# Performance work log

Hardware: AMD Instinct MI355X
Metric: run time of the kernel (lower is better)

The kernel has to match this reference:

```python
import jax, jax.numpy as jnp
import numpy as np

# Config derived from init_kwargs
DIM = 256
DSTATE = 64
DCONV = 3
HEADDIM = 64
CHUNK = 256
NGROUPS = 1
DINNER = int(2.0 * DIM)                 # 512
NHEADS = DINNER // HEADDIM              # 8
CONVDIM = DINNER + 2 * NGROUPS * DSTATE  # 640 (x, B, C share the depthwise conv)
DPROJ = 2 * DINNER + 2 * NGROUPS * DSTATE + NHEADS  # z + xBC + dt


def setup_inputs() -> dict:
    key = jax.random.key(0)
    ks = jax.random.split(key, 8)
    B, H, W = 8, 64, 64
    return dict(
        x=jax.random.normal(ks[0], (B, DIM, H, W), jnp.float32),
        ln_w=jnp.ones((DIM,), jnp.float32),
        ln_b=jnp.zeros((DIM,), jnp.float32),
        in_proj_w=jax.random.normal(ks[1], (DPROJ, DIM), jnp.float32) * 0.02,
        conv_w=jax.random.normal(ks[2], (CONVDIM, 1, DCONV, DCONV), jnp.float32) * 0.1,
        conv_b=jnp.zeros((CONVDIM,), jnp.float32),
        A_log=jnp.log(jax.random.uniform(ks[3], (NHEADS,), jnp.float32, 1.0, 16.0)),
        D=jnp.ones((NHEADS,), jnp.float32),
        dt_bias=jax.random.uniform(ks[4], (NHEADS,), jnp.float32, -2.0, 0.0),
        rms_w=jnp.ones((DINNER,), jnp.float32),
        out_proj_w=jax.random.normal(ks[5], (DIM, DINNER), jnp.float32) * 0.02,
    )


def _ssd(X, dA, Bm, Cm, chunk):
    """Mamba2 SSD chunked parallel scan.
    X:  (b, l, h, p)  inputs already multiplied by dt
    dA: (b, l, h)     dt * A (negative)
    Bm, Cm: (b, l, h, n)
    """
    b, l, h, p = X.shape
    n = Bm.shape[-1]
    c = l // chunk
    q = chunk
    Xc = X.reshape(b, c, q, h, p)
    Bc = Bm.reshape(b, c, q, h, n)
    Cc = Cm.reshape(b, c, q, h, n)
    Ac = dA.reshape(b, c, q, h).transpose(0, 3, 1, 2)            # (b,h,c,q)
    Acs = jnp.cumsum(Ac, axis=-1)                                # (b,h,c,q)
    # intra-chunk (diagonal blocks): causal decay matrix L
    tri = jnp.tril(jnp.ones((q, q), bool))
    Ldec = jnp.where(tri, jnp.exp(Acs[..., :, None] - Acs[..., None, :]), 0.0)
    Y_diag = jnp.einsum('bcqhn,bcshn,bhcqs,bcshp->bcqhp', Cc, Bc, Ldec, Xc)
    # per-chunk final states
    decay_states = jnp.exp(Acs[..., -1:] - Acs)                  # (b,h,c,q)
    states = jnp.einsum('bcqhn,bhcq,bcqhp->bchpn', Bc, decay_states, Xc)
    # inter-chunk recurrence (segment-sum over chunk totals)
    A_last = jnp.pad(Acs[..., -1], ((0, 0), (0, 0), (1, 0)))     # (b,h,c+1)
    ccs = jnp.cumsum(A_last, axis=-1)
    tric = jnp.tril(jnp.ones((c + 1, c + 1), bool))
    decay_chunk = jnp.where(tric, jnp.exp(ccs[..., :, None] - ccs[..., None, :]), 0.0)
    states0 = jnp.concatenate([jnp.zeros_like(states[:, :1]), states], axis=1)
    prev = jnp.einsum('bhzc,bchpn->bzhpn', decay_chunk, states0)[:, :-1]
    # contribution of carried-in state (off-diagonal blocks)
    Y_off = jnp.einsum('bcqhn,bchpn,bhcq->bcqhp', Cc, prev, jnp.exp(Acs))
    return (Y_diag + Y_off).reshape(b, l, h, p)


def _forward(x, ln_w, ln_b, in_proj_w, conv_w, conv_b, A_log, D, dt_bias, rms_w, out_proj_w):
    Bn, Cd, Hh, Ww = x.shape
    L = Hh * Ww
    # LayerNorm over channel dim (channel-first LayerNorm2d)
    mu = jnp.mean(x, axis=1, keepdims=True)
    var = jnp.mean((x - mu) ** 2, axis=1, keepdims=True)
    xn = (x - mu) * jax.lax.rsqrt(var + 1e-5)
    xn = xn * ln_w[None, :, None, None] + ln_b[None, :, None, None]
    # input projection (1x1): -> z | xBC | dt
    zxbcdt = jnp.einsum('bchw,dc->bdhw', xn, in_proj_w)
    z = zxbcdt[:, :DINNER]
    xBC = zxbcdt[:, DINNER:DINNER + CONVDIM]
    dt = zxbcdt[:, DINNER + CONVDIM:]                            # (b, nheads, H, W)
    # depthwise 2D conv + SiLU on xBC
    xBC = jax.lax.conv_general_dilated(
        xBC, conv_w, (1, 1), 'SAME',
        dimension_numbers=('NCHW', 'OIHW', 'NCHW'), feature_group_count=CONVDIM)
    xBC = jax.nn.silu(xBC + conv_b[None, :, None, None])
    # flatten spatial -> sequence, channel-last
    def to_seq(t):
        return t.reshape(Bn, t.shape[1], L).transpose(0, 2, 1)
    xBC, dt, z = to_seq(xBC), to_seq(dt), to_seq(z)
    xs = xBC[..., :DINNER].reshape(Bn, L, NHEADS, HEADDIM)
    Bg = xBC[..., DINNER:DINNER + NGROUPS * DSTATE].reshape(Bn, L, NGROUPS, DSTATE)
    Cg = xBC[..., DINNER + NGROUPS * DSTATE:].reshape(Bn, L, NGROUPS, DSTATE)
    hpg = NHEADS // NGROUPS
    Bm = jnp.repeat(Bg, hpg, axis=2)
    Cm = jnp.repeat(Cg, hpg, axis=2)
    dt = jax.nn.softplus(dt + dt_bias[None, None, :])            # (b, L, nheads)
    A = -jnp.exp(A_log)
    y = _ssd(xs * dt[..., None], dt * A[None, None, :], Bm, Cm, CHUNK)
    y = y + D[None, None, :, None] * xs                          # skip connection
    y = y.reshape(Bn, L, DINNER)
    # gated RMSNorm: norm(y * silu(z)) * w
    y = y * jax.nn.silu(z)
    y = y * jax.lax.rsqrt(jnp.mean(y * y, axis=-1, keepdims=True) + 1e-5) * rms_w
    out = jnp.einsum('bld,cd->blc', y, out_proj_w)
    out = out.transpose(0, 2, 1).reshape(Bn, Cd, Hh, Ww)
    return x + out                                               # residual


def reference(x, ln_w, ln_b, in_proj_w, conv_w, conv_b, A_log, D, dt_bias, rms_w, out_proj_w):
    return _forward(x, ln_w, ln_b, in_proj_w, conv_w, conv_b, A_log, D, dt_bias, rms_w, out_proj_w)
```

## Files before the change

### kernel.cpp

```cpp
#include <hip/hip_runtime.h>
#include <hip/hip_bf16.h>
#include <math.h>

#define DIMC   256
#define LSP    4096
#define BATCH  8
#define DINNER 512
#define NHEADS 8
#define HEADDIM 64
#define DSTATE 64
#define CONVDIM 640
#define DPROJ  1160
#define MPAD   1280
#define CHUNK  256
#define NCHUNK 16

typedef unsigned short u16;
typedef __attribute__((ext_vector_type(8))) unsigned short u16x8;
typedef __attribute__((ext_vector_type(8))) short s16x8;
typedef __attribute__((ext_vector_type(4))) float f32x4;

#define MFMA16(a,b,c) __builtin_amdgcn_mfma_f32_16x16x32_bf16((s16x8)(a),(s16x8)(b),(c),0,0,0)

__device__ __forceinline__ float bf2f(u16 u){ return __uint_as_float(((unsigned int)u)<<16); }
__device__ __forceinline__ u16 f2bf(float f){
  unsigned int x = __float_as_uint(f);
  unsigned int r = (x + 0x7fffu + ((x>>16)&1u)) >> 16;
  return (u16)r;
}
__device__ __forceinline__ float softplusf(float x){ return (x > 20.f) ? x : __logf(1.f + __expf(x)); }
__device__ __forceinline__ float siluf(float x){ return x * __builtin_amdgcn_rcpf(1.f + __expf(-x)); }

__global__ void convert_w(const float* __restrict__ src, u16* __restrict__ dst,
                          int total, int valid){
  int i = blockIdx.x*256 + threadIdx.x;
  if (i >= total) return;
  dst[i] = (i < valid) ? f2bf(src[i]) : (u16)0;
}

__global__ void convert_w_rms(const float* __restrict__ src, const float* __restrict__ rmsw,
                              u16* __restrict__ dst){
  int i = blockIdx.x*256 + threadIdx.x;
  if (i >= DIMC*DINNER) return;
  dst[i] = f2bf(src[i] * rmsw[i & (DINNER-1)]);
}

__global__ void ln_kernel(const float* __restrict__ X, const float* __restrict__ lnw,
                          const float* __restrict__ lnb, u16* __restrict__ XNT) {
  int pos = blockIdx.x*256 + threadIdx.x;
  int b = pos >> 12, l = pos & (LSP-1);
  const float* xb = X + ((size_t)b*DIMC)*LSP + l;
  float sum=0.f, sq=0.f;
  for (int c=0;c<DIMC;c++){ float v=xb[(size_t)c*LSP]; sum+=v; sq+=v*v; }
  float mu = sum*(1.f/DIMC);
  float var = sq*(1.f/DIMC) - mu*mu;
  float rs = rsqrtf(var + 1e-5f);
  u16* ob = XNT + ((size_t)(b*LSP + l))*DIMC;
  for (int c0=0;c0<DIMC;c0+=8){
    u16x8 v8;
    #pragma unroll
    for(int j=0;j<8;j++){
      float v = xb[(size_t)(c0+j)*LSP];
      v8[j] = f2bf((v-mu)*rs*lnw[c0+j] + lnb[c0+j]);
    }
    *(u16x8*)&ob[c0] = v8;
  }
}

__global__ __launch_bounds__(256,2) void gemm_in_fused(
    const u16* __restrict__ W, const u16* __restrict__ XNT,
    u16* __restrict__ ZT, u16* __restrict__ XBC, u16* __restrict__ DT){
  __shared__ u16 Xs[128][264];
  __shared__ u16 Ws[128][32];
  int tid=threadIdx.x, w=tid>>6, lane=tid&63, l15=lane&15, quad=lane>>4;
  int n0=blockIdx.x*128, mh=blockIdx.y, b=blockIdx.z;
  {
    const u16* src = XNT + ((size_t)(b*LSP + n0))*DIMC;
    #pragma unroll
    for (int i=0;i<16;i++){
      int g = i*256 + tid;
      int row = g>>5, c8 = (g&31)*8;
      *(u16x8*)&Xs[row][c8] = *(const u16x8*)&src[(size_t)row*DIMC + c8];
    }
  }
  for (int pti=0; pti<5; pti++){
    int ptg = mh*5 + pti;
    int m0 = ptg*128;
    f32x4 acc[4][4];
    #pragma unroll
    for(int i=0;i<4;i++)
      #pragma unroll
      for(int j=0;j<4;j++) acc[i][j]=(f32x4){0.f,0.f,0.f,0.f};
    for (int k0=0;k0<DIMC;k0+=32){
      __syncthreads();
      {
        int ch = tid*2;
        int r = ch>>2, o=(ch&3)*8;
        *(u16x8*)&Ws[r][o] = *(const u16x8*)&W[(size_t)(m0+r)*DIMC + k0 + o];
        ch++; r = ch>>2; o=(ch&3)*8;
        *(u16x8*)&Ws[r][o] = *(const u16x8*)&W[(size_t)(m0+r)*DIMC + k0 + o];
      }
      __syncthreads();
      u16x8 af[4], bfr[4];
      if (ptg < 4){
        #pragma unroll
        for(int mt=0;mt<4;mt++) af[mt] = *(const u16x8*)&Xs[(w>>1)*64+mt*16+l15][k0+quad*8];
        #pragma unroll
        for(int nt=0;nt<4;nt++) bfr[nt] = *(const u16x8*)&Ws[(w&1)*64+nt*16+l15][quad*8];
      } else {
        #pragma unroll
        for(int mt=0;mt<4;mt++) af[mt] = *(const u16x8*)&Ws[(w>>1)*64+mt*16+l15][quad*8];
        #pragma unroll
        for(int nt=0;nt<4;nt++) bfr[nt] = *(const u16x8*)&Xs[(w&1)*64+nt*16+l15][k0+quad*8];
      }
      #pragma unroll
      for(int mt=0;mt<4;mt++)
        #pragma unroll
        for(int nt=0;nt<4;nt++)
          acc[mt][nt]=MFMA16(af[mt],bfr[nt],acc[mt][nt]);
    }
    if (ptg < 4){
      #pragma unroll
      for(int mt=0;mt<4;mt++)
        #pragma unroll
        for(int nt=0;nt<4;nt++)
          #pragma unroll
          for(int r=0;r<4;r++){
            int lrow = n0 + (w>>1)*64 + mt*16 + quad*4 + r;
            int dcol = m0 + (w&1)*64 + nt*16 + l15;
            ZT[((size_t)b*LSP + lrow)*DINNER + dcol] = f2bf(acc[mt][nt][r]);
          }
    } else {
      #pragma unroll
      for(int mt=0;mt<4;mt++)
        #pragma unroll
        for(int nt=0;nt<4;nt++)
          #pragma unroll
          for(int r=0;r<4;r++){
            int prow = m0 + (w>>1)*64 + mt*16 + quad*4 + r;
            if (prow>=DPROJ) continue;
            int col = n0 + (w&1)*64 + nt*16 + l15;
            u16 v = f2bf(acc[mt][nt][r]);
            if (prow<DINNER+CONVDIM)  XBC[((size_t)b*CONVDIM+(prow-DINNER))*LSP+col]=v;
            else                      DT[((size_t)b*NHEADS+(prow-DINNER-CONVDIM))*LSP+col]=v;
          }
    }
  }
}

__global__ void gemm_out_mfma(const u16* __restrict__ A, const u16* __restrict__ Bm,
                              const float* __restrict__ Res, float* __restrict__ Out){
  __shared__ u16 As[128][32];
  __shared__ u16 Bs[128][32];
  __shared__ float rinv[128];
  int tid=threadIdx.x, w=tid>>6, lane=tid&63, l15=lane&15, quad=lane>>4;
  int b=blockIdx.z, m0=blockIdx.y*128, n0=blockIdx.x*128;
  const u16* Bb = Bm + ((size_t)b*LSP + n0)*DINNER;
  for (int rr=w; rr<128; rr+=4){
    u16x8 v = *(const u16x8*)&Bb[(size_t)rr*DINNER + lane*8];
    float s=0.f;
    #pragma unroll
    for(int j=0;j<8;j++){ float f=bf2f(v[j]); s+=f*f; }
    #pragma unroll
    for(int o=32;o>0;o>>=1) s += __shfl_xor(s,o,64);
    if (lane==0) rinv[rr] = rsqrtf(s*(1.f/DINNER) + 1e-5f);
  }
  f32x4 acc[4][4];
  #pragma unroll
  for(int i=0;i<4;i++)
    #pragma unroll
    for(int j=0;j<4;j++) acc[i][j] = (f32x4){0.f,0.f,0.f,0.f};
  for (int k0=0;k0<DINNER;k0+=32){
    __syncthreads();
    {
      int ch = tid*2;
      int r = ch>>2, o=(ch&3)*8;
      *(u16x8*)&As[r][o] = *(const u16x8*)&A[(size_t)(m0+r)*DINNER + k0 + o];
      *(u16x8*)&Bs[r][o] = *(const u16x8*)&Bb[(size_t)r*DINNER + k0 + o];
      ch++; r = ch>>2; o=(ch&3)*8;
      *(u16x8*)&As[r][o] = *(const u16x8*)&A[(size_t)(m0+r)*DINNER + k0 + o];
      *(u16x8*)&Bs[r][o] = *(const u16x8*)&Bb[(size_t)r*DINNER + k0 + o];
    }
    __syncthreads();
    u16x8 af[4], bfr[4];
    #pragma unroll
    for(int mt=0;mt<4;mt++) af[mt] = *(const u16x8*)&As[(w>>1)*64+mt*16+l15][quad*8];
    #pragma unroll
    for(int nt=0;nt<4;nt++) bfr[nt] = *(const u16x8*)&Bs[(w&1)*64+nt*16+l15][quad*8];
    #pragma unroll
    for(int mt=0;mt<4;mt++)
      #pragma unroll
      for(int nt=0;nt<4;nt++)
        acc[mt][nt]=MFMA16(af[mt],bfr[nt],acc[mt][nt]);
  }
  #pragma unroll
  for(int mt=0;mt<4;mt++)
    #pragma unroll
    for(int nt=0;nt<4;nt++){
      float rv = rinv[(w&1)*64 + nt*16 + l15];
      #pragma unroll
      for(int r=0;r<4;r++){
        int row = m0 + (w>>1)*64 + mt*16 + quad*4 + r;
        int col = n0 + (w&1)*64 + nt*16 + l15;
        size_t oi = ((size_t)b*DIMC+row)*LSP+col;
        Out[oi] = acc[mt][nt][r]*rv + Res[oi];
      }
    }
}

__global__ void conv_kernel(u16* __restrict__ XBC, const float* __restrict__ CW,
                            const float* __restrict__ CB){
  int ch = blockIdx.x, b = blockIdx.y, tid = threadIdx.x;
  __shared__ float plane[66*66];
  u16* base = XBC + ((size_t)b*CONVDIM + ch)*LSP;
  for (int idx=tid; idx<66*66; idx+=256){
    int yy = idx/66 - 1, xx = idx%66 - 1;
    float v = 0.f;
    if (yy>=0 && yy<64 && xx>=0 && xx<64) v = bf2f(base[yy*64+xx]);
    plane[idx] = v;
  }
  float wg[9];
  #pragma unroll
  for (int t=0;t<9;t++) wg[t] = CW[ch*9+t];
  float bias = CB[ch];
  __syncthreads();
  for (int r=0;r<16;r++){
    int pix = tid + r*256;
    int y = pix>>6, x = pix&63;
    float s=0.f;
    #pragma unroll
    for(int dy=0;dy<3;dy++)
      #pragma unroll
      for(int dx=0;dx<3;dx++) s += plane[(y+dy)*66 + x+dx]*wg[dy*3+dx];
    base[pix] = f2bf(siluf(s + bias));
  }
}

__global__ void ssd_pre_kernel(const u16* __restrict__ DT, const float* __restrict__ A_log,
                               const float* __restrict__ dt_bias, float* __restrict__ ACS,
                               float* __restrict__ DTV, float* __restrict__ DASUM){
  int c=blockIdx.x, h=blockIdx.y, b=blockIdx.z, tid=threadIdx.x;
  __shared__ float acs[CHUNK];
  size_t base = ((size_t)b*NHEADS+h)*LSP + c*CHUNK + tid;
  float raw = bf2f(DT[base]);
  float dtv = softplusf(raw + dt_bias[h]);
  float Ah = -__expf(A_log[h]);
  acs[tid] = dtv*Ah;
  __syncthreads();
  for(int o=1;o<256;o<<=1){
    float add=(tid>=o)?acs[tid-o]:0.f;
    __syncthreads(); acs[tid]+=add; __syncthreads();
  }
  ACS[base] = acs[tid];
  DTV[base] = dtv;
  if (tid==CHUNK-1) DASUM[((size_t)b*NHEADS+h)*NCHUNK+c] = acs[tid];
}

__global__ __launch_bounds__(256,4) void ssd_states_mfma(
    const float* __restrict__ ACS, const float* __restrict__ DTV,
    const float* __restrict__ DASUM, const u16* __restrict__ XBC,
    float* __restrict__ STATES){
  int c=blockIdx.x, h=blockIdx.y, b=blockIdx.z;
  int tid=threadIdx.x, w=tid>>6, lane=tid&63, l15=lane&15, quad=lane>>4;
  __shared__ float wdt[CHUNK];
  __shared__ u16 Xw[64][136];
  __shared__ u16 Bn[64][136];
  {
    size_t base = ((size_t)b*NHEADS+h)*LSP + c*CHUNK + tid;
    float atot = DASUM[((size_t)b*NHEADS+h)*NCHUNK+c];
    wdt[tid] = DTV[base]*__expf(atot - ACS[base]);
  }
  __syncthreads();
  f32x4 acc[4];
  #pragma unroll
  for(int i=0;i<4;i++) acc[i] = (f32x4){0.f,0.f,0.f,0.f};
  size_t cb = (size_t)c*CHUNK;
  for(int th=0; th<2; th++){
    __syncthreads();
    {
      int n=tid&63, q4=tid>>6;
      const u16* Xg = XBC + ((size_t)b*CONVDIM + h*HEADDIM + n)*LSP + cb + th*128;
      const u16* Bg = XBC + ((size_t)b*CONVDIM + DINNER + n)*LSP + cb + th*128;
      #pragma unroll
      for(int i=0;i<4;i++){
        int o = q4*32+i*8;
        u16x8 v = *(const u16x8*)&Xg[o];
        u16x8 wv;
        #pragma unroll
        for(int j=0;j<8;j++) wv[j]=f2bf(bf2f(v[j])*wdt[th*128+o+j]);
        *(u16x8*)&Xw[n][o]=wv;
        *(u16x8*)&Bn[n][o] = *(const u16x8*)&Bg[o];
      }
    }
    __syncthreads();
    #pragma unroll
    for(int k8=0;k8<4;k8++){
      u16x8 a = *(const u16x8*)&Xw[w*16+l15][k8*32+quad*8];
      #pragma unroll
      for(int nt=0;nt<4;nt++){
        u16x8 bb = *(const u16x8*)&Bn[nt*16+l15][k8*32+quad*8];
        acc[nt]=MFMA16(a,bb,acc[nt]);
      }
    }
  }
  float* dst = STATES + (((size_t)b*NHEADS+h)*NCHUNK+c)*4096;
  #pragma unroll
  for(int nt=0;nt<4;nt++)
    #pragma unroll
    for(int r=0;r<4;r++)
      dst[(w*16+quad*4+r)*64 + nt*16+l15] = acc[nt][r];
}

__global__ void ssd_scan_kernel(const float* __restrict__ STATES, const float* __restrict__ DASUM,
                                u16* __restrict__ PREVB){
  int g = blockIdx.x, h = blockIdx.y, b = blockIdx.z, tid = threadIdx.x;
  int e = g*256 + tid;
  size_t hb = (size_t)b*NHEADS + h;
  size_t base = hb*NCHUNK*4096 + e;
  float s = 0.f;
  for (int cc=0;cc<NCHUNK;cc++){
    PREVB[base + (size_t)cc*4096] = f2bf(s);
    s = s*__expf(DASUM[hb*NCHUNK + cc]) + STATES[base + (size_t)cc*4096];
  }
}

__global__ __launch_bounds__(256,4) void ssd_y_mfma(
    const float* __restrict__ ACS, const float* __restrict__ DTV,
    const u16* __restrict__ XBC, const float* __restrict__ Dp,
    const u16* __restrict__ PREVB, const u16* __restrict__ ZT,
    u16* __restrict__ YG){
  int bx = blockIdx.x; int c = bx>>2, tb = bx&3;
  int h = blockIdx.y, b = blockIdx.z;
  int tid=threadIdx.x, w=tid>>6, lane=tid&63, l15=lane&15, quad=lane>>4;
  __shared__ float acs[CHUNK];
  __shared__ float dtv[CHUNK];
  __shared__ u16 Ct[64][72];
  __shared__ u16 Bsb[64][72];
  __shared__ u16 Xsb[64][72];
  __shared__ u16 P[4][16][72];
  {
    size_t base = ((size_t)b*NHEADS+h)*LSP + c*CHUNK + tid;
    acs[tid] = ACS[base];
    dtv[tid] = DTV[base];
  }
  {
    int n = tid&63, q4 = tid>>6;
    const u16* Cg = XBC + ((size_t)b*CONVDIM + DINNER + DSTATE + n)*LSP + (size_t)c*CHUNK + tb*64;
    #pragma unroll
    for(int i=0;i<2;i++){
      u16x8 v = *(const u16x8*)&Cg[q4*16+i*8];
      #pragma unroll
      for(int j=0;j<8;j++) Ct[q4*16+i*8+j][n]=v[j];
    }
  }
  __syncthreads();
  f32x4 Yd[4], Yo[4];
  #pragma unroll
  for(int i=0;i<4;i++){ Yd[i]=(f32x4){0.f,0.f,0.f,0.f}; Yo[i]=(f32x4){0.f,0.f,0.f,0.f}; }
  int trow = w*16 + l15;
  u16x8 ca0 = *(const u16x8*)&Ct[trow][quad*8];
  u16x8 ca1 = *(const u16x8*)&Ct[trow][32+quad*8];
  {
    const u16* Pg = PREVB + (((size_t)b*NHEADS+h)*NCHUNK + c)*4096;
    #pragma unroll
    for(int pt=0;pt<4;pt++){
      u16x8 b0 = *(const u16x8*)&Pg[(pt*16+l15)*64 + quad*8];
      u16x8 b1 = *(const u16x8*)&Pg[(pt*16+l15)*64 + 32 + quad*8];
      Yo[pt]=MFMA16(ca0,b0,Yo[pt]);
      Yo[pt]=MFMA16(ca1,b1,Yo[pt]);
    }
  }
  int tloc = tb*64 + w*16 + quad*4;
  float acst[4];
  #pragma unroll
  for(int r=0;r<4;r++) acst[r] = acs[tloc+r];
  float Dh = Dp[h];
  for(int sb=0; sb<=tb; sb++){
    __syncthreads();
    {
      int n=tid&63, q4=tid>>6;
      const u16* Bg = XBC + ((size_t)b*CONVDIM + DINNER + n)*LSP + (size_t)c*CHUNK + sb*64;
      #pragma unroll
      for(int i=0;i<2;i++){
        u16x8 v = *(const u16x8*)&Bg[q4*16+i*8];
        #pragma unroll
        for(int j=0;j<8;j++) Bsb[q4*16+i*8+j][n]=v[j];
      }
      const u16* Xg = XBC + ((size_t)b*CONVDIM + h*HEADDIM + n)*LSP + (size_t)c*CHUNK + sb*64;
      #pragma unroll
      for(int i=0;i<2;i++){
        int o = q4*16+i*8;
        *(u16x8*)&Xsb[n][o] = *(const u16x8*)&Xg[o];
      }
    }
    __syncthreads();
    f32x4 S[4];
    #pragma unroll
    for(int st=0;st<4;st++){
      S[st]=(f32x4){0.f,0.f,0.f,0.f};
      u16x8 b0 = *(const u16x8*)&Bsb[st*16+l15][quad*8];
      u16x8 b1 = *(const u16x8*)&Bsb[st*16+l15][32+quad*8];
      S[st]=MFMA16(ca0,b0,S[st]);
      S[st]=MFMA16(ca1,b1,S[st]);
    }
    if (sb < tb){
      #pragma unroll
      for(int st=0;st<4;st++){
        int s = sb*64 + st*16 + l15;
        float as = acs[s], dv = dtv[s];
        #pragma unroll
        for(int r=0;r<4;r++)
          P[w][quad*4+r][st*16+l15] = f2bf(S[st][r]*__expf(acst[r]-as)*dv);
      }
    } else {
      #pragma unroll
      for(int st=0;st<4;st++){
        int s = sb*64 + st*16 + l15;
        float as = acs[s], dv = dtv[s];
        #pragma unroll
        for(int r=0;r<4;r++){
          int t = tloc + r;
          float pv;
          if (s < t)       pv = S[st][r]*__expf(acst[r]-as)*dv;
          else if (s == t) pv = S[st][r]*dv + Dh;
          else             pv = 0.f;
          P[w][quad*4+r][st*16+l15] = f2bf(pv);
        }
      }
    }
    u16x8 p0 = *(const u16x8*)&P[w][l15][quad*8];
    u16x8 p1 = *(const u16x8*)&P[w][l15][32+quad*8];
    #pragma unroll
    for(int pt=0;pt<4;pt++){
      u16x8 x0 = *(const u16x8*)&Xsb[pt*16+l15][quad*8];
      u16x8 x1 = *(const u16x8*)&Xsb[pt*16+l15][32+quad*8];
      Yd[pt]=MFMA16(p0,x0,Yd[pt]);
      Yd[pt]=MFMA16(p1,x1,Yd[pt]);
    }
  }
  float eat[4];
  #pragma unroll
  for(int r=0;r<4;r++) eat[r] = __expf(acst[r]);
  size_t lbase = (size_t)b*LSP + c*CHUNK + tb*64;
  #pragma unroll
  for(int pt=0;pt<4;pt++){
    #pragma unroll
    for(int r=0;r<4;r++){
      int tl = w*16 + quad*4 + r;
      int p = pt*16 + l15;
      float y = Yd[pt][r] + eat[r]*Yo[pt][r];
      size_t oi = (lbase + tl)*DINNER + h*HEADDIM + p;
      float zv = bf2f(ZT[oi]);
      YG[oi] = f2bf(y * siluf(zv));
    }
  }
}

extern "C" void kernel_launch(void* const* d_in, const int* in_sizes, int n_in,
                              void* d_out, int out_size, void* d_ws, size_t ws_size,
                              hipStream_t stream) {
  const float* x     = (const float*)d_in[0];
  const float* lnw   = (const float*)d_in[1];
  const float* lnb   = (const float*)d_in[2];
  const float* inpw  = (const float*)d_in[3];
  const float* convw = (const float*)d_in[4];
  const float* convb = (const float*)d_in[5];
  const float* alog  = (const float*)d_in[6];
  const float* Dp    = (const float*)d_in[7];
  const float* dtbi  = (const float*)d_in[8];
  const float* rmsw  = (const float*)d_in[9];
  const float* outw  = (const float*)d_in[10];
  float* out = (float*)d_out;

  char* ws = (char*)d_ws;
  size_t off = 0;
  auto alloc = [&](size_t bytes)->void*{ void* p = ws+off; off += (bytes+255)&~(size_t)255; return p; };
  u16*   WPIN   = (u16*)  alloc((size_t)MPAD*DIMC*2);
  u16*   WPOUT  = (u16*)  alloc((size_t)DIMC*DINNER*2);
  char*  RA     = (char*) alloc((size_t)BATCH*NHEADS*NCHUNK*4096*4);
  u16*   XNT    = (u16*)RA;
  float* STATES = (float*)RA;
  u16*   ZT     = (u16*)  alloc((size_t)BATCH*LSP*DINNER*2);
  u16*   XBC    = (u16*)  alloc((size_t)BATCH*CONVDIM*LSP*2);
  u16*   DTb    = (u16*)  alloc((size_t)BATCH*NHEADS*LSP*2);
  u16*   PREVB  = (u16*)  alloc((size_t)BATCH*NHEADS*NCHUNK*4096*2);
  float* DASUM  = (float*)alloc((size_t)BATCH*NHEADS*NCHUNK*4);
  float* ACS    = (float*)alloc((size_t)BATCH*NHEADS*LSP*4);
  float* DTV    = (float*)alloc((size_t)BATCH*NHEADS*LSP*4);
  u16*   YG     = (u16*)  alloc((size_t)BATCH*LSP*DINNER*2);

  convert_w<<<(MPAD*DIMC+255)/256,256,0,stream>>>(inpw, WPIN, MPAD*DIMC, DPROJ*DIMC);
  convert_w_rms<<<(DIMC*DINNER+255)/256,256,0,stream>>>(outw, rmsw, WPOUT);
  ln_kernel<<<dim3(BATCH*LSP/256),256,0,stream>>>(x,lnw,lnb,XNT);
  gemm_in_fused<<<dim3(LSP/128,2,BATCH),256,0,stream>>>(WPIN, XNT, ZT, XBC, DTb);
  conv_kernel<<<dim3(CONVDIM,BATCH),256,0,stream>>>(XBC, convw, convb);
  ssd_pre_kernel<<<dim3(NCHUNK,NHEADS,BATCH),256,0,stream>>>(DTb, alog, dtbi, ACS, DTV, DASUM);
  ssd_states_mfma<<<dim3(NCHUNK,NHEADS,BATCH),256,0,stream>>>(ACS,DTV,DASUM,XBC,STATES);
  ssd_scan_kernel<<<dim3(16,NHEADS,BATCH),256,0,stream>>>(STATES,DASUM,PREVB);
  ssd_y_mfma<<<dim3(NCHUNK*4,NHEADS,BATCH),256,0,stream>>>(ACS,DTV,XBC,Dp,PREVB,ZT,YG);
  gemm_out_mfma<<<dim3(LSP/128,DIMC/128,BATCH),256,0,stream>>>(WPOUT, YG, x, out);
}
```

Baseline: 350.6 us.

## Transpose B/C once into token-major buffer and read MFMA operands directly from global

Adds a kernel that transposes the B and C rows of XBC into a token-major BCT buffer. The SSD y kernel then loads its C, B and X MFMA fragments straight from global memory instead of staging them through shared memory with per-block scalar transposes and barriers. The states kernel likewise drops its shared-memory staging. Occupancy hints are raised on both kernels. The trade is an extra pass over B/C plus uncoalesced-looking strided global fragment loads that rely on the cache, in exchange for fewer barriers and less LDS traffic.

Result: slower. 444.4 us (+26.8%).

```diff
diff --git a/kernel.cpp b/kernel.cpp
--- a/kernel.cpp
+++ b/kernel.cpp
@@ -233,6 +233,27 @@
       #pragma unroll
       for(int dx=0;dx<3;dx++) s += plane[(y+dy)*66 + x+dx]*wg[dy*3+dx];
     base[pix] = f2bf(siluf(s + bias));
+  }
+}
+
+__global__ void xpose_bc(const u16* __restrict__ XBC, u16* __restrict__ BCT){
+  int lb = blockIdx.x, b = blockIdx.y, tid = threadIdx.x;
+  __shared__ u16 T[64][136];
+  int l0 = lb*64;
+  #pragma unroll
+  for(int i=0;i<4;i++){
+    int idx = i*256 + tid;
+    int n = idx>>3, l8 = (idx&7)*8;
+    u16x8 v = *(const u16x8*)&XBC[((size_t)b*CONVDIM + DINNER + n)*LSP + l0 + l8];
+    #pragma unroll
+    for(int j=0;j<8;j++) T[l8+j][n] = v[j];
+  }
+  __syncthreads();
+  #pragma unroll
+  for(int i=0;i<4;i++){
+    int idx = i*256 + tid;
+    int l = idx>>4, n8 = (idx&15)*8;
+    *(u16x8*)&BCT[((size_t)(b*LSP + l0 + l))*128 + n8] = *(const u16x8*)&T[l][n8];
   }
 }
 
@@ -256,15 +277,13 @@
   if (tid==CHUNK-1) DASUM[((size_t)b*NHEADS+h)*NCHUNK+c] = acs[tid];
 }
 
-__global__ __launch_bounds__(256,4) void ssd_states_mfma(
+__global__ __launch_bounds__(256,8) void ssd_states_mfma(
     const float* __restrict__ ACS, const float* __restrict__ DTV,
     const float* __restrict__ DASUM, const u16* __restrict__ XBC,
     float* __restrict__ STATES){
   int c=blockIdx.x, h=blockIdx.y, b=blockIdx.z;
   int tid=threadIdx.x, w=tid>>6, lane=tid&63, l15=lane&15, quad=lane>>4;
   __shared__ float wdt[CHUNK];
-  __shared__ u16 Xw[64][136];
-  __shared__ u16 Bn[64][136];
   {
     size_t base = ((size_t)b*NHEADS+h)*LSP + c*CHUNK + tid;
     float atot = DASUM[((size_t)b*NHEADS+h)*NCHUNK+c];
@@ -275,32 +294,18 @@
   #pragma unroll
   for(int i=0;i<4;i++) acc[i] = (f32x4){0.f,0.f,0.f,0.f};
   size_t cb = (size_t)c*CHUNK;
-  for(int th=0; th<2; th++){
-    __syncthreads();
-    {
-      int n=tid&63, q4=tid>>6;
-      const u16* Xg = XBC + ((size_t)b*CONVDIM + h*HEADDIM + n)*LSP + cb + th*128;
-      const u16* Bg = XBC + ((size_t)b*CONVDIM + DINNER + n)*LSP + cb + th*128;
-      #pragma unroll
-      for(int i=0;i<4;i++){
-        int o = q4*32+i*8;
-        u16x8 v = *(const u16x8*)&Xg[o];
-        u16x8 wv;
-        #pragma unroll
-        for(int j=0;j<8;j++) wv[j]=f2bf(bf2f(v[j])*wdt[th*128+o+j]);
-        *(u16x8*)&Xw[n][o]=wv;
-        *(u16x8*)&Bn[n][o] = *(const u16x8*)&Bg[o];
-      }
-    }
-    __syncthreads();
-    #pragma unroll
-    for(int k8=0;k8<4;k8++){
-      u16x8 a = *(const u16x8*)&Xw[w*16+l15][k8*32+quad*8];
-      #pragma unroll
-      for(int nt=0;nt<4;nt++){
-        u16x8 bb = *(const u16x8*)&Bn[nt*16+l15][k8*32+quad*8];
-        acc[nt]=MFMA16(a,bb,acc[nt]);
-      }
+  const u16* Xrow = XBC + ((size_t)b*CONVDIM + h*HEADDIM + w*16 + l15)*LSP + cb;
+  #pragma unroll
+  for(int k32=0;k32<8;k32++){
+    int t0 = k32*32 + quad*8;
+    u16x8 xv = *(const u16x8*)&Xrow[t0];
+    u16x8 a;
+    #pragma unroll
+    for(int j=0;j<8;j++) a[j] = f2bf(bf2f(xv[j]) * wdt[t0+j]);
+    #pragma unroll
+    for(int nt=0;nt<4;nt++){
+      u16x8 bb = *(const u16x8*)&XBC[((size_t)b*CONVDIM + DINNER + nt*16+l15)*LSP + cb + t0];
+      acc[nt]=MFMA16(a,bb,acc[nt]);
     }
   }
   float* dst = STATES + (((size_t)b*NHEADS+h)*NCHUNK+c)*4096;
@@ -324,42 +329,31 @@
   }
 }
 
-__global__ __launch_bounds__(256,4) void ssd_y_mfma(
+__global__ __launch_bounds__(256,6) void ssd_y_mfma(
     const float* __restrict__ ACS, const float* __restrict__ DTV,
-    const u16* __restrict__ XBC, const float* __restrict__ Dp,
-    const u16* __restrict__ PREVB, const u16* __restrict__ ZT,
-    u16* __restrict__ YG){
+    const u16* __restrict__ XBC, const u16* __restrict__ BCT,
+    const float* __restrict__ Dp, const u16* __restrict__ PREVB,
+    const u16* __restrict__ ZT, u16* __restrict__ YG){
   int bx = blockIdx.x; int c = bx>>2, tb = bx&3;
   int h = blockIdx.y, b = blockIdx.z;
   int tid=threadIdx.x, w=tid>>6, lane=tid&63, l15=lane&15, quad=lane>>4;
   __shared__ float acs[CHUNK];
   __shared__ float dtv[CHUNK];
-  __shared__ u16 Ct[64][72];
-  __shared__ u16 Bsb[64][72];
-  __shared__ u16 Xsb[64][72];
   __shared__ u16 P[4][16][72];
   {
     size_t base = ((size_t)b*NHEADS+h)*LSP + c*CHUNK + tid;
     acs[tid] = ACS[base];
     dtv[tid] = DTV[base];
   }
-  {
-    int n = tid&63, q4 = tid>>6;
-    const u16* Cg = XBC + ((size_t)b*CONVDIM + DINNER + DSTATE + n)*LSP + (size_t)c*CHUNK + tb*64;
-    #pragma unroll
-    for(int i=0;i<2;i++){
-      u16x8 v = *(const u16x8*)&Cg[q4*16+i*8];
-      #pragma unroll
-      for(int j=0;j<8;j++) Ct[q4*16+i*8+j][n]=v[j];
-    }
-  }
   __syncthreads();
+  size_t lchunk = (size_t)b*LSP + (size_t)c*CHUNK;
+  int trow = w*16 + l15;
+  const u16* Crow = BCT + (lchunk + tb*64 + trow)*128 + 64;
+  u16x8 ca0 = *(const u16x8*)&Crow[quad*8];
+  u16x8 ca1 = *(const u16x8*)&Crow[32+quad*8];
   f32x4 Yd[4], Yo[4];
   #pragma unroll
   for(int i=0;i<4;i++){ Yd[i]=(f32x4){0.f,0.f,0.f,0.f}; Yo[i]=(f32x4){0.f,0.f,0.f,0.f}; }
-  int trow = w*16 + l15;
-  u16x8 ca0 = *(const u16x8*)&Ct[trow][quad*8];
-  u16x8 ca1 = *(const u16x8*)&Ct[trow][32+quad*8];
   {
     const u16* Pg = PREVB + (((size_t)b*NHEADS+h)*NCHUNK + c)*4096;
     #pragma unroll
@@ -375,31 +369,15 @@
   #pragma unroll
   for(int r=0;r<4;r++) acst[r] = acs[tloc+r];
   float Dh = Dp[h];
+  const u16* Xbase = XBC + ((size_t)b*CONVDIM + h*HEADDIM)*LSP + (size_t)c*CHUNK;
   for(int sb=0; sb<=tb; sb++){
-    __syncthreads();
-    {
-      int n=tid&63, q4=tid>>6;
-      const u16* Bg = XBC + ((size_t)b*CONVDIM + DINNER + n)*LSP + (size_t)c*CHUNK + sb*64;
-      #pragma unroll
-      for(int i=0;i<2;i++){
-        u16x8 v = *(const u16x8*)&Bg[q4*16+i*8];
-        #pragma unroll
-        for(int j=0;j<8;j++) Bsb[q4*16+i*8+j][n]=v[j];
-      }
-      const u16* Xg = XBC + ((size_t)b*CONVDIM + h*HEADDIM + n)*LSP + (size_t)c*CHUNK + sb*64;
-      #pragma unroll
-      for(int i=0;i<2;i++){
-        int o = q4*16+i*8;
-        *(u16x8*)&Xsb[n][o] = *(const u16x8*)&Xg[o];
-      }
-    }
-    __syncthreads();
     f32x4 S[4];
     #pragma unroll
     for(int st=0;st<4;st++){
       S[st]=(f32x4){0.f,0.f,0.f,0.f};
-      u16x8 b0 = *(const u16x8*)&Bsb[st*16+l15][quad*8];
-      u16x8 b1 = *(const u16x8*)&Bsb[st*16+l15][32+quad*8];
+      const u16* Brow = BCT + (lchunk + sb*64 + st*16 + l15)*128;
+      u16x8 b0 = *(const u16x8*)&Brow[quad*8];
+      u16x8 b1 = *(const u16x8*)&Brow[32+quad*8];
       S[st]=MFMA16(ca0,b0,S[st]);
       S[st]=MFMA16(ca1,b1,S[st]);
     }
@@ -432,8 +410,9 @@
     u16x8 p1 = *(const u16x8*)&P[w][l15][32+quad*8];
     #pragma unroll
     for(int pt=0;pt<4;pt++){
-      u16x8 x0 = *(const u16x8*)&Xsb[pt*16+l15][quad*8];
-      u16x8 x1 = *(const u16x8*)&Xsb[pt*16+l15][32+quad*8];
+      const u16* Xrow = Xbase + (size_t)(pt*16+l15)*LSP + sb*64;
+      u16x8 x0 = *(const u16x8*)&Xrow[quad*8];
+      u16x8 x1 = *(const u16x8*)&Xrow[32+quad*8];
       Yd[pt]=MFMA16(p0,x0,Yd[pt]);
       Yd[pt]=MFMA16(p1,x1,Yd[pt]);
     }
@@ -441,7 +420,7 @@
   float eat[4];
   #pragma unroll
   for(int r=0;r<4;r++) eat[r] = __expf(acst[r]);
-  size_t lbase = (size_t)b*LSP + c*CHUNK + tb*64;
+  size_t lbase = lchunk + tb*64;
   #pragma unroll
   for(int pt=0;pt<4;pt++){
     #pragma unroll
@@ -484,6 +463,7 @@
   u16*   XBC    = (u16*)  alloc((size_t)BATCH*CONVDIM*LSP*2);
   u16*   DTb    = (u16*)  alloc((size_t)BATCH*NHEADS*LSP*2);
   u16*   PREVB  = (u16*)  alloc((size_t)BATCH*NHEADS*NCHUNK*4096*2);
+  u16*   BCT    = (u16*)  alloc((size_t)BATCH*LSP*128*2);
   float* DASUM  = (float*)alloc((size_t)BATCH*NHEADS*NCHUNK*4);
   float* ACS    = (float*)alloc((size_t)BATCH*NHEADS*LSP*4);
   float* DTV    = (float*)alloc((size_t)BATCH*NHEADS*LSP*4);
@@ -494,9 +474,10 @@
   ln_kernel<<<dim3(BATCH*LSP/256),256,0,stream>>>(x,lnw,lnb,XNT);
   gemm_in_fused<<<dim3(LSP/128,2,BATCH),256,0,stream>>>(WPIN, XNT, ZT, XBC, DTb);
   conv_kernel<<<dim3(CONVDIM,BATCH),256,0,stream>>>(XBC, convw, convb);
+  xpose_bc<<<dim3(LSP/64,BATCH),256,0,stream>>>(XBC, BCT);
   ssd_pre_kernel<<<dim3(NCHUNK,NHEADS,BATCH),256,0,stream>>>(DTb, alog, dtbi, ACS, DTV, DASUM);
   ssd_states_mfma<<<dim3(NCHUNK,NHEADS,BATCH),256,0,stream>>>(ACS,DTV,DASUM,XBC,STATES);
   ssd_scan_kernel<<<dim3(16,NHEADS,BATCH),256,0,stream>>>(STATES,DASUM,PREVB);
-  ssd_y_mfma<<<dim3(NCHUNK*4,NHEADS,BATCH),256,0,stream>>>(ACS,DTV,XBC,Dp,PREVB,ZT,YG);
+  ssd_y_mfma<<<dim3(NCHUNK*4,NHEADS,BATCH),256,0,stream>>>(ACS,DTV,XBC,BCT,Dp,PREVB,ZT,YG);
   gemm_out_mfma<<<dim3(LSP/128,DIMC/128,BATCH),256,0,stream>>>(WPOUT, YG, x, out);
 }
```
